# Performance work log

Measured on AMD Instinct MI355X. Metric: run time of the kernel, lower is better.

Reference implementation:

```python
import jax, jax.numpy as jnp
import numpy as np

TOP_K = 2


def setup_inputs() -> dict:
    key = jax.random.key(0)
    k1, k2, k3, k4 = jax.random.split(key, 4)
    B, T, D = 1, 2048, 1024
    E, F = 8, 2048
    scale_in = 1.0 / np.sqrt(D)
    scale_f = 1.0 / np.sqrt(F)
    x = jax.random.normal(k1, (B, T, D), dtype=jnp.float32)
    Wr = jax.random.normal(k2, (E, D), dtype=jnp.float32) * scale_in  # router weight [E, D]
    W1 = jax.random.normal(k3, (E, F, D), dtype=jnp.float32) * scale_in  # fc1 weights stacked [E, F, D]
    W2 = jax.random.normal(k4, (E, D, F), dtype=jnp.float32) * scale_f  # fc2 weights stacked [E, D, F]
    return {"x": x, "Wr": Wr, "W1": W1, "W2": W2}


def reference(x, Wr, W1, W2):
    B, T, D = x.shape
    E = Wr.shape[0]
    xf = x.reshape(B * T, D)  # [N, D]
    N = xf.shape[0]

    # Router: softmax over experts, top-k gating, renormalized
    logits = xf @ Wr.T  # [N, E]
    probs = jax.nn.softmax(logits, axis=-1)
    top_vals, top_idx = jax.lax.top_k(probs, TOP_K)  # [N, K]
    top_vals = top_vals / jnp.sum(top_vals, axis=-1, keepdims=True)

    # Dense per-token gate matrix: gates[n, e] = sum_k top_vals[n,k] * (top_idx[n,k]==e)
    gates = jnp.zeros((N, E), dtype=x.dtype).at[
        jnp.arange(N)[:, None], top_idx
    ].add(top_vals)  # [N, E]

    # Expert MLP: fc2(relu(fc1(x))^2), computed densely for all experts then
    # combined with the (mostly-zero) gate weights.
    h = jnp.einsum("nd,efd->nef", xf, W1)  # [N, E, F]
    a = jnp.square(jax.nn.relu(h))
    y = jnp.einsum("nef,edf->ned", a, W2)  # [N, E, D]
    out = jnp.einsum("ne,ned->nd", gates, y)  # [N, D]
    return out.reshape(B, T, D)
```

## Files before the change

kernel.cpp:

```cpp
#include <hip/hip_runtime.h>
#include <hip/hip_bf16.h>
#include <cstdint>
#include <cstddef>

#define N_TOK 2048
#define DIM   1024
#define NEXP  8
#define FDIM  2048

#define BM 128
#define BN 128
#define BK 64

typedef __attribute__((ext_vector_type(8))) short short8;
typedef __attribute__((ext_vector_type(4))) float f32x4;
typedef __attribute__((ext_vector_type(2))) unsigned int uint2v;
typedef unsigned short ushort_t;

#define OFF_COUNTS  0
#define OFF_TOK     4096
#define OFF_GATE    (OFF_TOK + NEXP * N_TOK * 4)
#define OFF_A       ((size_t)1 << 20)
#define OFF_W1B     (OFF_A  + (size_t)2 * N_TOK * FDIM * 2)
#define OFF_W2B     (OFF_W1B + (size_t)NEXP * FDIM * DIM * 2)
#define OFF_XB      (OFF_W2B + (size_t)NEXP * DIM * FDIM * 2)

__device__ __forceinline__ uint32_t cvt2(float lo, float hi) {
  __hip_bfloat162 p = __float22bfloat162_rn(make_float2(lo, hi));
  uint32_t r; __builtin_memcpy(&r, &p, 4); return r;
}

__device__ __forceinline__ void gl16(const ushort_t* g, const ushort_t* l) {
  __builtin_amdgcn_global_load_lds(
      (const __attribute__((address_space(1))) void*)g,
      (__attribute__((address_space(3))) void*)l, 16, 0, 0);
}

__device__ __forceinline__ int xcd_swz(int bid, int nwg) {
  int q = nwg >> 3, r = nwg & 7;
  int xcd = bid & 7, local = bid >> 3;
  int base = (xcd < r) ? xcd * (q + 1) : r * (q + 1) + (xcd - r) * q;
  return base + local;
}

__global__ __launch_bounds__(256) void prep_kernel(
    const float* __restrict__ W1, const float* __restrict__ W2, const float* __restrict__ x,
    ushort_t* __restrict__ W1b, ushort_t* __restrict__ W2b, ushort_t* __restrict__ xb) {
  int b = blockIdx.x;
  const f32x4* s; uint2v* d; size_t off;
  if (b < 2048)      { s = (const f32x4*)W1; d = (uint2v*)W1b; off = (size_t)b * 2048; }
  else if (b < 4096) { s = (const f32x4*)W2; d = (uint2v*)W2b; off = (size_t)(b - 2048) * 2048; }
  else               { s = (const f32x4*)x;  d = (uint2v*)xb;  off = (size_t)(b - 4096) * 2048; }
  s += off; d += off;
  int tid = threadIdx.x;
  f32x4 v[8];
#pragma unroll
  for (int k = 0; k < 8; ++k) v[k] = __builtin_nontemporal_load(&s[tid + k * 256]);
#pragma unroll
  for (int k = 0; k < 8; ++k) {
    uint2v o; o.x = cvt2(v[k].x, v[k].y); o.y = cvt2(v[k].z, v[k].w);
    d[tid + k * 256] = o;
  }
}

__global__ __launch_bounds__(256) void router_kernel(
    const float* __restrict__ x, const float* __restrict__ Wr,
    int* __restrict__ counts, int* __restrict__ toklist,
    float* __restrict__ gatelist) {
  int n = blockIdx.x * 4 + (threadIdx.x >> 6);
  int lane = threadIdx.x & 63;
  const float* xr = x + (size_t)n * DIM;

  float xv[DIM / 64];
#pragma unroll
  for (int i = 0; i < DIM / 64; ++i) xv[i] = xr[lane + 64 * i];

  float logit[NEXP];
#pragma unroll
  for (int e = 0; e < NEXP; ++e) {
    const float* wr = Wr + (size_t)e * DIM;
    float s = 0.f;
#pragma unroll
    for (int i = 0; i < DIM / 64; ++i) s += xv[i] * wr[lane + 64 * i];
#pragma unroll
    for (int off = 32; off; off >>= 1) s += __shfl_down(s, off);
    logit[e] = s;
  }

  if (lane == 0) {
    float m = logit[0];
#pragma unroll
    for (int e = 1; e < NEXP; ++e) m = fmaxf(m, logit[e]);
    float p[NEXP];
#pragma unroll
    for (int e = 0; e < NEXP; ++e) p[e] = expf(logit[e] - m);
    int i1 = 0;
#pragma unroll
    for (int e = 1; e < NEXP; ++e) if (p[e] > p[i1]) i1 = e;
    int i2 = (i1 == 0) ? 1 : 0;
#pragma unroll
    for (int e = 0; e < NEXP; ++e)
      if (e != i1 && p[e] > p[i2]) i2 = e;
    float denom = p[i1] + p[i2];

    int pos1 = atomicAdd(&counts[i1], 1);
    toklist[i1 * N_TOK + pos1] = n;
    gatelist[i1 * N_TOK + pos1] = p[i1] / denom;

    int pos2 = atomicAdd(&counts[i2], 1);
    toklist[i2 * N_TOK + pos2] = n;
    gatelist[i2 * N_TOK + pos2] = p[i2] / denom;
  }
}

__global__ __launch_bounds__(256, 2) void fc1_mfma(
    const ushort_t* __restrict__ xb, const ushort_t* __restrict__ W1b,
    const int* __restrict__ counts, const int* __restrict__ toklist,
    __hip_bfloat16* __restrict__ Abuf) {
  const int ROWB = N_TOK / BM;
  const int COLB = FDIM / BN;
  int bid = xcd_swz(blockIdx.x, NEXP * ROWB * COLB);
  int e  = bid / (ROWB * COLB);
  int rb = (bid / COLB) % ROWB;
  int cb = bid % COLB;
  int ne = counts[e];
  if (rb * BM >= ne) return;
  int base = 0;
  for (int i = 0; i < e; ++i) base += counts[i];

  __shared__ ushort_t As[2][BM * BK];
  __shared__ ushort_t Bs[2][BN * BK];

  int tid = threadIdx.x, lane = tid & 63, w = tid >> 6;

  const ushort_t* gA[4]; const ushort_t* gB[4];
#pragma unroll
  for (int i = 0; i < 4; ++i) {
    int row = w * 32 + i * 8 + (lane >> 3);
    int c16 = (lane & 7) ^ (row & 7);
    int r = rb * BM + row; if (r >= ne) r = ne - 1;
    int tok = toklist[e * N_TOK + r];
    gA[i] = xb + (size_t)tok * DIM + c16 * 8;
    gB[i] = W1b + ((size_t)e * FDIM + cb * BN + row) * DIM + c16 * 8;
  }

  int wr = (w >> 1) * 64, wc = (w & 1) * 64;
  int lr = lane & 15, lg = lane >> 4;
  f32x4 acc[4][4] = {};

#define ISSUE(buf, t) do { _Pragma("unroll") for (int i = 0; i < 4; ++i) { \
    gl16(gA[i] + (size_t)(t) * BK, &As[buf][w * 2048 + i * 512]); \
    gl16(gB[i] + (size_t)(t) * BK, &Bs[buf][w * 2048 + i * 512]); } } while (0)

  const int NT = DIM / BK;
  asm volatile("s_waitcnt vmcnt(0)" ::: "memory");
  ISSUE(0, 0);
  for (int t = 0; t < NT; ++t) {
    int cur = t & 1;
    if (t + 1 < NT) {
      ISSUE(cur ^ 1, t + 1);
      asm volatile("s_waitcnt vmcnt(8)" ::: "memory");
    } else {
      asm volatile("s_waitcnt vmcnt(0)" ::: "memory");
    }
    __builtin_amdgcn_sched_barrier(0);
    __builtin_amdgcn_s_barrier();
#pragma unroll
    for (int ks = 0; ks < 2; ++ks) {
      short8 af[4], bf[4];
#pragma unroll
      for (int m = 0; m < 4; ++m) {
        int row = wr + m * 16 + lr;
        af[m] = *(const short8*)&As[cur][row * BK + (((ks * 4 + lg) ^ (row & 7)) * 8)];
      }
#pragma unroll
      for (int n = 0; n < 4; ++n) {
        int row = wc + n * 16 + lr;
        bf[n] = *(const short8*)&Bs[cur][row * BK + (((ks * 4 + lg) ^ (row & 7)) * 8)];
      }
#pragma unroll
      for (int m = 0; m < 4; ++m)
#pragma unroll
        for (int n = 0; n < 4; ++n)
          acc[m][n] = __builtin_amdgcn_mfma_f32_16x16x32_bf16(af[m], bf[n], acc[m][n], 0, 0, 0);
    }
    asm volatile("s_waitcnt lgkmcnt(0)" ::: "memory");
    __builtin_amdgcn_sched_barrier(0);
    __builtin_amdgcn_s_barrier();
  }
#undef ISSUE

  int colbase = cb * BN + wc + lr;
#pragma unroll
  for (int m = 0; m < 4; ++m) {
#pragma unroll
    for (int j = 0; j < 4; ++j) {
      int r = rb * BM + wr + m * 16 + lg * 4 + j;
      if (r < ne) {
        __hip_bfloat16* orow = Abuf + (size_t)(base + r) * FDIM + colbase;
#pragma unroll
        for (int n = 0; n < 4; ++n) {
          float v = fmaxf(acc[m][n][j], 0.f);
          orow[n * 16] = __float2bfloat16(v * v);
        }
      }
    }
  }
}

__global__ __launch_bounds__(256, 2) void fc2_mfma(
    const ushort_t* __restrict__ Abuf, const ushort_t* __restrict__ W2b,
    const int* __restrict__ counts, const int* __restrict__ toklist,
    const float* __restrict__ gatelist, float* __restrict__ out) {
  const int ROWB = N_TOK / BM;
  const int COLB = DIM / BN;
  int bid = xcd_swz(blockIdx.x, NEXP * ROWB * COLB);
  int e  = bid / (ROWB * COLB);
  int rb = (bid / COLB) % ROWB;
  int cb = bid % COLB;
  int ks0 = blockIdx.y * (FDIM / 2);
  int ne = counts[e];
  if (rb * BM >= ne) return;
  int base = 0;
  for (int i = 0; i < e; ++i) base += counts[i];

  __shared__ ushort_t As[2][BM * BK];
  __shared__ ushort_t Bs[2][BN * BK];

  int tid = threadIdx.x, lane = tid & 63, w = tid >> 6;

  const ushort_t* gA[4]; const ushort_t* gB[4];
#pragma unroll
  for (int i = 0; i < 4; ++i) {
    int row = w * 32 + i * 8 + (lane >> 3);
    int c16 = (lane & 7) ^ (row & 7);
    int r = rb * BM + row; if (r >= ne) r = ne - 1;
    gA[i] = Abuf + (size_t)(base + r) * FDIM + ks0 + c16 * 8;
    gB[i] = W2b + ((size_t)e * DIM + cb * BN + row) * FDIM + ks0 + c16 * 8;
  }

  int wr = (w >> 1) * 64, wc = (w & 1) * 64;
  int lr = lane & 15, lg = lane >> 4;
  f32x4 acc[4][4] = {};

#define ISSUE(buf, t) do { _Pragma("unroll") for (int i = 0; i < 4; ++i) { \
    gl16(gA[i] + (size_t)(t) * BK, &As[buf][w * 2048 + i * 512]); \
    gl16(gB[i] + (size_t)(t) * BK, &Bs[buf][w * 2048 + i * 512]); } } while (0)

  const int NT = (FDIM / 2) / BK;
  asm volatile("s_waitcnt vmcnt(0)" ::: "memory");
  ISSUE(0, 0);
  for (int t = 0; t < NT; ++t) {
    int cur = t & 1;
    if (t + 1 < NT) {
      ISSUE(cur ^ 1, t + 1);
      asm volatile("s_waitcnt vmcnt(8)" ::: "memory");
    } else {
      asm volatile("s_waitcnt vmcnt(0)" ::: "memory");
    }
    __builtin_amdgcn_sched_barrier(0);
    __builtin_amdgcn_s_barrier();
#pragma unroll
    for (int ks = 0; ks < 2; ++ks) {
      short8 af[4], bf[4];
#pragma unroll
      for (int m = 0; m < 4; ++m) {
        int row = wr + m * 16 + lr;
        af[m] = *(const short8*)&As[cur][row * BK + (((ks * 4 + lg) ^ (row & 7)) * 8)];
      }
#pragma unroll
      for (int n = 0; n < 4; ++n) {
        int row = wc + n * 16 + lr;
        bf[n] = *(const short8*)&Bs[cur][row * BK + (((ks * 4 + lg) ^ (row & 7)) * 8)];
      }
#pragma unroll
      for (int m = 0; m < 4; ++m)
#pragma unroll
        for (int n = 0; n < 4; ++n)
          acc[m][n] = __builtin_amdgcn_mfma_f32_16x16x32_bf16(af[m], bf[n], acc[m][n], 0, 0, 0);
    }
    asm volatile("s_waitcnt lgkmcnt(0)" ::: "memory");
    __builtin_amdgcn_sched_barrier(0);
    __builtin_amdgcn_s_barrier();
  }
#undef ISSUE

  int colbase = cb * BN + wc + lr;
#pragma unroll
  for (int m = 0; m < 4; ++m) {
#pragma unroll
    for (int j = 0; j < 4; ++j) {
      int r = rb * BM + wr + m * 16 + lg * 4 + j;
      if (r < ne) {
        int tok = toklist[e * N_TOK + r];
        float g = gatelist[e * N_TOK + r];
        float* orow = out + (size_t)tok * DIM + colbase;
#pragma unroll
        for (int n = 0; n < 4; ++n)
          atomicAdd(&orow[n * 16], g * acc[m][n][j]);
      }
    }
  }
}

extern "C" void kernel_launch(void* const* d_in, const int* in_sizes, int n_in,
                              void* d_out, int out_size, void* d_ws, size_t ws_size,
                              hipStream_t stream) {
  const float* x  = (const float*)d_in[0];
  const float* Wr = (const float*)d_in[1];
  const float* W1 = (const float*)d_in[2];
  const float* W2 = (const float*)d_in[3];
  float* out = (float*)d_out;

  char* ws = (char*)d_ws;
  int*   counts   = (int*)(ws + OFF_COUNTS);
  int*   toklist  = (int*)(ws + OFF_TOK);
  float* gatelist = (float*)(ws + OFF_GATE);
  __hip_bfloat16* Abuf = (__hip_bfloat16*)(ws + OFF_A);
  ushort_t* W1b = (ushort_t*)(ws + OFF_W1B);
  ushort_t* W2b = (ushort_t*)(ws + OFF_W2B);
  ushort_t* xb  = (ushort_t*)(ws + OFF_XB);

  (void)hipMemsetAsync(counts, 0, NEXP * sizeof(int), stream);
  (void)hipMemsetAsync(out, 0, (size_t)out_size * sizeof(float), stream);

  prep_kernel<<<4352, 256, 0, stream>>>(W1, W2, x, W1b, W2b, xb);

  router_kernel<<<N_TOK / 4, 256, 0, stream>>>(x, Wr, counts, toklist, gatelist);

  fc1_mfma<<<NEXP * (N_TOK / BM) * (FDIM / BN), 256, 0, stream>>>(
      xb, W1b, counts, toklist, Abuf);

  fc2_mfma<<<dim3(NEXP * (N_TOK / BM) * (DIM / BN), 2), 256, 0, stream>>>(
      (const ushort_t*)Abuf, W2b, counts, toklist, gatelist, out);
}
```

Measured before the change: 307.0 us.

## Halve GEMM K-tile to raise occupancy and fold memsets into prep kernel

```diff
diff --git a/kernel.cpp b/kernel.cpp
--- a/kernel.cpp
+++ b/kernel.cpp
@@ -10,7 +10,7 @@
 
 #define BM 128
 #define BN 128
-#define BK 64
+#define BK 32
 
 typedef __attribute__((ext_vector_type(8))) short short8;
 typedef __attribute__((ext_vector_type(4))) float f32x4;
@@ -45,14 +45,26 @@
 
 __global__ __launch_bounds__(256) void prep_kernel(
     const float* __restrict__ W1, const float* __restrict__ W2, const float* __restrict__ x,
-    ushort_t* __restrict__ W1b, ushort_t* __restrict__ W2b, ushort_t* __restrict__ xb) {
+    ushort_t* __restrict__ W1b, ushort_t* __restrict__ W2b, ushort_t* __restrict__ xb,
+    float* __restrict__ out, int* __restrict__ counts) {
   int b = blockIdx.x;
+  int tid = threadIdx.x;
+  if (b >= 4352) {
+    if (b == 4608) {
+      if (tid < NEXP) counts[tid] = 0;
+      return;
+    }
+    f32x4* o = (f32x4*)out + (size_t)(b - 4352) * 2048;
+    f32x4 z = {0.f, 0.f, 0.f, 0.f};
+#pragma unroll
+    for (int k = 0; k < 8; ++k) o[tid + k * 256] = z;
+    return;
+  }
   const f32x4* s; uint2v* d; size_t off;
   if (b < 2048)      { s = (const f32x4*)W1; d = (uint2v*)W1b; off = (size_t)b * 2048; }
   else if (b < 4096) { s = (const f32x4*)W2; d = (uint2v*)W2b; off = (size_t)(b - 2048) * 2048; }
   else               { s = (const f32x4*)x;  d = (uint2v*)xb;  off = (size_t)(b - 4096) * 2048; }
   s += off; d += off;
-  int tid = threadIdx.x;
   f32x4 v[8];
 #pragma unroll
   for (int k = 0; k < 8; ++k) v[k] = __builtin_nontemporal_load(&s[tid + k * 256]);
@@ -113,7 +125,7 @@
   }
 }
 
-__global__ __launch_bounds__(256, 2) void fc1_mfma(
+__global__ __launch_bounds__(256, 4) void fc1_mfma(
     const ushort_t* __restrict__ xb, const ushort_t* __restrict__ W1b,
     const int* __restrict__ counts, const int* __restrict__ toklist,
     __hip_bfloat16* __restrict__ Abuf) {
@@ -133,24 +145,24 @@
 
   int tid = threadIdx.x, lane = tid & 63, w = tid >> 6;
 
-  const ushort_t* gA[4]; const ushort_t* gB[4];
-#pragma unroll
-  for (int i = 0; i < 4; ++i) {
-    int row = w * 32 + i * 8 + (lane >> 3);
-    int c16 = (lane & 7) ^ (row & 7);
+  const ushort_t* gA[2]; const ushort_t* gB[2];
+#pragma unroll
+  for (int i = 0; i < 2; ++i) {
+    int row = w * 32 + i * 16 + (lane >> 2);
+    int sl  = (lane & 3) ^ (row & 3);
     int r = rb * BM + row; if (r >= ne) r = ne - 1;
     int tok = toklist[e * N_TOK + r];
-    gA[i] = xb + (size_t)tok * DIM + c16 * 8;
-    gB[i] = W1b + ((size_t)e * FDIM + cb * BN + row) * DIM + c16 * 8;
+    gA[i] = xb + (size_t)tok * DIM + sl * 8;
+    gB[i] = W1b + ((size_t)e * FDIM + cb * BN + row) * DIM + sl * 8;
   }
 
   int wr = (w >> 1) * 64, wc = (w & 1) * 64;
   int lr = lane & 15, lg = lane >> 4;
   f32x4 acc[4][4] = {};
 
-#define ISSUE(buf, t) do { _Pragma("unroll") for (int i = 0; i < 4; ++i) { \
-    gl16(gA[i] + (size_t)(t) * BK, &As[buf][w * 2048 + i * 512]); \
-    gl16(gB[i] + (size_t)(t) * BK, &Bs[buf][w * 2048 + i * 512]); } } while (0)
+#define ISSUE(buf, t) do { _Pragma("unroll") for (int i = 0; i < 2; ++i) { \
+    gl16(gA[i] + (size_t)(t) * BK, &As[buf][w * 1024 + i * 512]); \
+    gl16(gB[i] + (size_t)(t) * BK, &Bs[buf][w * 1024 + i * 512]); } } while (0)
 
   const int NT = DIM / BK;
   asm volatile("s_waitcnt vmcnt(0)" ::: "memory");
@@ -159,24 +171,23 @@
     int cur = t & 1;
     if (t + 1 < NT) {
       ISSUE(cur ^ 1, t + 1);
-      asm volatile("s_waitcnt vmcnt(8)" ::: "memory");
+      asm volatile("s_waitcnt vmcnt(4)" ::: "memory");
     } else {
       asm volatile("s_waitcnt vmcnt(0)" ::: "memory");
     }
     __builtin_amdgcn_sched_barrier(0);
     __builtin_amdgcn_s_barrier();
-#pragma unroll
-    for (int ks = 0; ks < 2; ++ks) {
+    {
       short8 af[4], bf[4];
 #pragma unroll
       for (int m = 0; m < 4; ++m) {
         int row = wr + m * 16 + lr;
-        af[m] = *(const short8*)&As[cur][row * BK + (((ks * 4 + lg) ^ (row & 7)) * 8)];
+        af[m] = *(const short8*)&As[cur][row * BK + ((lg ^ (row & 3)) * 8)];
       }
 #pragma unroll
       for (int n = 0; n < 4; ++n) {
         int row = wc + n * 16 + lr;
-        bf[n] = *(const short8*)&Bs[cur][row * BK + (((ks * 4 + lg) ^ (row & 7)) * 8)];
+        bf[n] = *(const short8*)&Bs[cur][row * BK + ((lg ^ (row & 3)) * 8)];
       }
 #pragma unroll
       for (int m = 0; m < 4; ++m)
@@ -208,7 +219,7 @@
   }
 }
 
-__global__ __launch_bounds__(256, 2) void fc2_mfma(
+__global__ __launch_bounds__(256, 4) void fc2_mfma(
     const ushort_t* __restrict__ Abuf, const ushort_t* __restrict__ W2b,
     const int* __restrict__ counts, const int* __restrict__ toklist,
     const float* __restrict__ gatelist, float* __restrict__ out) {
@@ -229,23 +240,23 @@
 
   int tid = threadIdx.x, lane = tid & 63, w = tid >> 6;
 
-  const ushort_t* gA[4]; const ushort_t* gB[4];
-#pragma unroll
-  for (int i = 0; i < 4; ++i) {
-    int row = w * 32 + i * 8 + (lane >> 3);
-    int c16 = (lane & 7) ^ (row & 7);
+  const ushort_t* gA[2]; const ushort_t* gB[2];
+#pragma unroll
+  for (int i = 0; i < 2; ++i) {
+    int row = w * 32 + i * 16 + (lane >> 2);
+    int sl  = (lane & 3) ^ (row & 3);
     int r = rb * BM + row; if (r >= ne) r = ne - 1;
-    gA[i] = Abuf + (size_t)(base + r) * FDIM + ks0 + c16 * 8;
-    gB[i] = W2b + ((size_t)e * DIM + cb * BN + row) * FDIM + ks0 + c16 * 8;
+    gA[i] = Abuf + (size_t)(base + r) * FDIM + ks0 + sl * 8;
+    gB[i] = W2b + ((size_t)e * DIM + cb * BN + row) * FDIM + ks0 + sl * 8;
   }
 
   int wr = (w >> 1) * 64, wc = (w & 1) * 64;
   int lr = lane & 15, lg = lane >> 4;
   f32x4 acc[4][4] = {};
 
-#define ISSUE(buf, t) do { _Pragma("unroll") for (int i = 0; i < 4; ++i) { \
-    gl16(gA[i] + (size_t)(t) * BK, &As[buf][w * 2048 + i * 512]); \
-    gl16(gB[i] + (size_t)(t) * BK, &Bs[buf][w * 2048 + i * 512]); } } while (0)
+#define ISSUE(buf, t) do { _Pragma("unroll") for (int i = 0; i < 2; ++i) { \
+    gl16(gA[i] + (size_t)(t) * BK, &As[buf][w * 1024 + i * 512]); \
+    gl16(gB[i] + (size_t)(t) * BK, &Bs[buf][w * 1024 + i * 512]); } } while (0)
 
   const int NT = (FDIM / 2) / BK;
   asm volatile("s_waitcnt vmcnt(0)" ::: "memory");
@@ -254,24 +265,23 @@
     int cur = t & 1;
     if (t + 1 < NT) {
       ISSUE(cur ^ 1, t + 1);
-      asm volatile("s_waitcnt vmcnt(8)" ::: "memory");
+      asm volatile("s_waitcnt vmcnt(4)" ::: "memory");
     } else {
       asm volatile("s_waitcnt vmcnt(0)" ::: "memory");
     }
     __builtin_amdgcn_sched_barrier(0);
     __builtin_amdgcn_s_barrier();
-#pragma unroll
-    for (int ks = 0; ks < 2; ++ks) {
+    {
       short8 af[4], bf[4];
 #pragma unroll
       for (int m = 0; m < 4; ++m) {
         int row = wr + m * 16 + lr;
-        af[m] = *(const short8*)&As[cur][row * BK + (((ks * 4 + lg) ^ (row & 7)) * 8)];
+        af[m] = *(const short8*)&As[cur][row * BK + ((lg ^ (row & 3)) * 8)];
       }
 #pragma unroll
       for (int n = 0; n < 4; ++n) {
         int row = wc + n * 16 + lr;
-        bf[n] = *(const short8*)&Bs[cur][row * BK + (((ks * 4 + lg) ^ (row & 7)) * 8)];
+        bf[n] = *(const short8*)&Bs[cur][row * BK + ((lg ^ (row & 3)) * 8)];
       }
 #pragma unroll
       for (int m = 0; m < 4; ++m)
@@ -321,10 +331,7 @@
   ushort_t* W2b = (ushort_t*)(ws + OFF_W2B);
   ushort_t* xb  = (ushort_t*)(ws + OFF_XB);
 
-  (void)hipMemsetAsync(counts, 0, NEXP * sizeof(int), stream);
-  (void)hipMemsetAsync(out, 0, (size_t)out_size * sizeof(float), stream);
-
-  prep_kernel<<<4352, 256, 0, stream>>>(W1, W2, x, W1b, W2b, xb);
+  prep_kernel<<<4609, 256, 0, stream>>>(W1, W2, x, W1b, W2b, xb, out, counts);
 
   router_kernel<<<N_TOK / 4, 256, 0, stream>>>(x, Wr, counts, toklist, gatelist);
 
```

Result: faster. 290.6 us (-5.4%).
